# Optimization experiments

Hardware: AMD Instinct MI355X
Metric: run time of the kernel (lower is better)

The kernel has to match this reference:

```python
import jax, jax.numpy as jnp
import numpy as np

N_NODES, D, B, NEG2, DRUG_NUM = 20000, 512, 2048, 64, 2000
H1, H2 = 128, 64


def setup_inputs() -> dict:
    ks = jax.random.split(jax.random.key(0), 10)
    embed = jax.random.normal(ks[0], (N_NODES, D), dtype=jnp.float32)
    h = jax.random.randint(ks[1], (B, 1), 0, DRUG_NUM)
    t = jax.random.randint(ks[2], (B, 1), 0, N_NODES)
    n_s = jax.random.randint(ks[3], (B, NEG2), 0, DRUG_NUM)  # all < drug_num -> chunk branch
    s1 = 1.0 / np.sqrt(2 * D)
    s2 = 1.0 / np.sqrt(H1)
    s3 = 1.0 / np.sqrt(H2)
    W1 = jax.random.uniform(ks[4], (2 * D, H1), minval=-s1, maxval=s1, dtype=jnp.float32)
    b1 = jax.random.uniform(ks[5], (H1,), minval=-s1, maxval=s1, dtype=jnp.float32)
    W2 = jax.random.uniform(ks[6], (H1, H2), minval=-s2, maxval=s2, dtype=jnp.float32)
    b2 = jax.random.uniform(ks[7], (H2,), minval=-s2, maxval=s2, dtype=jnp.float32)
    W3 = jax.random.uniform(ks[8], (H2, 1), minval=-s3, maxval=s3, dtype=jnp.float32)
    b3 = jax.random.uniform(ks[9], (1,), minval=-s3, maxval=s3, dtype=jnp.float32)
    return {"embed": embed, "W1": W1, "b1": b1, "W2": W2, "b2": b2, "W3": W3, "b3": b3,
            "h": h, "t": t, "n_s": n_s}


def _mlp(x, W1, b1, W2, b2, W3, b3):
    # [..., 2D] -> [...] score
    x = jax.nn.relu(x @ W1 + b1)
    x = jax.nn.relu(x @ W2 + b2)
    return (x @ W3 + b3)[..., 0]


def reference(embed, W1, b1, W2, b2, W3, b3, h, t, n_s):
    K = n_s.shape[1] // 2
    n_t, n_h = n_s[:, :K], n_s[:, K:]
    h_e = embed[h]          # [B, 1, D]
    t_e = embed[t]          # [B, T, D]
    T = t.shape[1]
    # positive pairs: [B, T]
    pos = _mlp(jnp.concatenate([jnp.tile(h_e, (1, T, 1)), t_e], axis=-1),
               W1, b1, W2, b2, W3, b3)
    # corrupted-tail negatives: [B, K]
    neg1 = _mlp(jnp.concatenate([jnp.tile(h_e, (1, K, 1)), embed[n_t]], axis=-1),
                W1, b1, W2, b2, W3, b3)
    # corrupted-head negatives: [B, T*K] (T=1 here)
    neg2 = _mlp(jnp.concatenate([embed[n_h], jnp.tile(t_e, (1, K, 1))], axis=-1),
                W1, b1, W2, b2, W3, b3)
    neg = jnp.concatenate([neg1, neg2], axis=1)  # [B, 2K]
    return pos, neg
```

## Files before the change

kernel.cpp:

```cpp
#include <hip/hip_runtime.h>

#define DIM    512
#define BATCH  2048
#define NDRUG  2000
#define H1     128
#define H2     64
#define NITEM  65
#define SLAB   774144
#define W2F_OFF  (SLAB)
#define W1F_OFF  (W2F_OFF + 4096)
#define LP       65

typedef __attribute__((ext_vector_type(8))) short short8;
typedef __attribute__((ext_vector_type(4))) float floatx4;

__device__ inline unsigned f2bf(float x) {
    union { float f; unsigned u; } v; v.f = x;
    unsigned r = v.u + 0x7fffu + ((v.u >> 16) & 1u);
    return r >> 16;
}
__device__ inline unsigned pkbf(float a, float b) {
    return f2bf(a) | (f2bf(b) << 16);
}
__device__ inline short8 cvt8(const float* __restrict__ src) {
    float4 a = *(const float4*)src, b = *(const float4*)(src + 4);
    union { short8 s; unsigned u[4]; } v;
    v.u[0] = pkbf(a.x, a.y); v.u[1] = pkbf(a.z, a.w);
    v.u[2] = pkbf(b.x, b.y); v.u[3] = pkbf(b.z, b.w);
    return v.s;
}

__global__ __launch_bounds__(256) void pack_w(
    const float* __restrict__ W1, const float* __restrict__ W2,
    float* __restrict__ ws)
{
    const int blk = blockIdx.x, tid = threadIdx.x;
    if (blk < 64) {
        short8* W1f = (short8*)(ws + W1F_OFF);
        int item = blk * 256 + tid;
        int frag = item >> 6, lane = item & 63;
        int half = frag >> 7, kt = (frag >> 3) & 15, nt = frag & 7;
        int n = lane & 15, q = lane >> 4;
        short8 v;
        #pragma unroll
        for (int j = 0; j < 8; ++j) {
            int k = half * DIM + kt * 32 + q * 8 + j;
            v[j] = (short)f2bf(W1[k * H1 + nt * 16 + n]);
        }
        W1f[item] = v;
    } else {
        short8* W2f = (short8*)(ws + W2F_OFF);
        #pragma unroll
        for (int i = 0; i < 4; ++i) {
            int item = i * 256 + tid;
            int frag = item >> 6, lane = item & 63;
            int kt = frag >> 2, nt = frag & 3;
            int n = lane & 15, q = lane >> 4;
            short8 v;
            #pragma unroll
            for (int j = 0; j < 8; ++j)
                v[j] = (short)f2bf(W2[(kt * 32 + q * 8 + j) * H2 + nt * 16 + n]);
            W2f[item] = v;
        }
    }
}

__global__ __launch_bounds__(256) void layer1(
    const float* __restrict__ embed, const float* __restrict__ b1,
    const int* __restrict__ t, float* __restrict__ ws)
{
    __shared__ short8 ldsA[16 * LP];
    const short8* W1f = (const short8*)(ws + W1F_OFF);
    const int blk = blockIdx.x, tid = threadIdx.x;
    const bool isPQ = blk < 125;
    const int rowbase = isPQ ? blk * 16 : (blk - 125) * 16;

    #pragma unroll
    for (int i = 0; i < 4; ++i) {
        int u = i * 256 + tid;
        int r = u >> 6, c = u & 63;
        size_t grow = isPQ ? (size_t)(rowbase + r) : (size_t)t[rowbase + r];
        ldsA[r * LP + c] = cvt8(embed + grow * DIM + c * 8);
    }
    __syncthreads();

    const int lane = tid & 63, wv = tid >> 6;
    const int n = lane & 15, q = lane >> 4;

    if (isPQ) {
        const int T0 = wv * 4;
        const int half = (T0 >= 8) ? 1 : 0;
        floatx4 acc[4];
        #pragma unroll
        for (int i = 0; i < 4; ++i) acc[i] = (floatx4){0.f, 0.f, 0.f, 0.f};
        #pragma unroll
        for (int kt = 0; kt < 16; ++kt) {
            short8 a = ldsA[n * LP + kt * 4 + q];
            #pragma unroll
            for (int i = 0; i < 4; ++i) {
                int nt = (T0 + i) & 7;
                short8 bf = W1f[(size_t)(((half * 16 + kt) * 8) + nt) * 64 + lane];
                acc[i] = __builtin_amdgcn_mfma_f32_16x16x32_bf16(a, bf, acc[i], 0, 0, 0);
            }
        }
        float* tbl = ws + (half ? NDRUG * H1 : 0);
        #pragma unroll
        for (int i = 0; i < 4; ++i) {
            int nt = (T0 + i) & 7;
            float badd = half ? b1[nt * 16 + n] : 0.f;
            #pragma unroll
            for (int reg = 0; reg < 4; ++reg)
                tbl[(size_t)(rowbase + q * 4 + reg) * H1 + nt * 16 + n] =
                    acc[i][reg] + badd;
        }
    } else {
        const int T0 = wv * 2;
        floatx4 acc[2];
        #pragma unroll
        for (int i = 0; i < 2; ++i) acc[i] = (floatx4){0.f, 0.f, 0.f, 0.f};
        #pragma unroll
        for (int kt = 0; kt < 16; ++kt) {
            short8 a = ldsA[n * LP + kt * 4 + q];
            #pragma unroll
            for (int i = 0; i < 2; ++i) {
                int nt = T0 + i;
                short8 bf = W1f[(size_t)(((16 + kt) * 8) + nt) * 64 + lane];
                acc[i] = __builtin_amdgcn_mfma_f32_16x16x32_bf16(a, bf, acc[i], 0, 0, 0);
            }
        }
        float* tbl = ws + 2 * (NDRUG * H1);
        #pragma unroll
        for (int i = 0; i < 2; ++i) {
            int nt = T0 + i;
            float badd = b1[nt * 16 + n];
            #pragma unroll
            for (int reg = 0; reg < 4; ++reg)
                tbl[(size_t)(rowbase + q * 4 + reg) * H1 + nt * 16 + n] =
                    acc[i][reg] + badd;
        }
    }
}

__global__ __launch_bounds__(256) void score_mfma(
    const float* __restrict__ ws,
    const float* __restrict__ b2, const float* __restrict__ W3,
    const float* __restrict__ b3,
    const int* __restrict__ h, const int* __restrict__ ns,
    float* __restrict__ out)
{
    const float* P  = ws;
    const float* Q  = ws + NDRUG * H1;
    const float* Qt = Q + NDRUG * H1;
    const short8* W2f = (const short8*)(ws + W2F_OFF);

    const int lane = threadIdx.x & 63;
    const int wv   = threadIdx.x >> 6;
    const int tile = blockIdx.x * 4 + wv;
    const int n = lane & 15, q = lane >> 4;

    const int sg   = tile * 16 + n;
    const int b    = sg / NITEM;
    const int item = sg - b * NITEM;
    const float *Pr, *Qr;
    if (item == 0)       { Pr = P + h[b] * H1;                        Qr = Qt + b * H1; }
    else if (item <= 32) { Pr = P + h[b] * H1;                        Qr = Q + ns[b * 64 + item - 1] * H1; }
    else                 { Pr = P + ns[b * 64 + 32 + item - 33] * H1; Qr = Qt + b * H1; }

    floatx4 acc[4];
    #pragma unroll
    for (int nt = 0; nt < 4; ++nt) acc[nt] = (floatx4){0.f, 0.f, 0.f, 0.f};

    #pragma unroll
    for (int kt = 0; kt < 4; ++kt) {
        const int kb = kt * 32 + q * 8;
        float4 p0 = *(const float4*)(Pr + kb);
        float4 p1 = *(const float4*)(Pr + kb + 4);
        float4 q0 = *(const float4*)(Qr + kb);
        float4 q1 = *(const float4*)(Qr + kb + 4);
        union { short8 s; unsigned u[4]; } A;
        A.u[0] = pkbf(fmaxf(p0.x + q0.x, 0.f), fmaxf(p0.y + q0.y, 0.f));
        A.u[1] = pkbf(fmaxf(p0.z + q0.z, 0.f), fmaxf(p0.w + q0.w, 0.f));
        A.u[2] = pkbf(fmaxf(p1.x + q1.x, 0.f), fmaxf(p1.y + q1.y, 0.f));
        A.u[3] = pkbf(fmaxf(p1.z + q1.z, 0.f), fmaxf(p1.w + q1.w, 0.f));
        #pragma unroll
        for (int nt = 0; nt < 4; ++nt) {
            short8 bf = W2f[(kt * 4 + nt) * 64 + lane];
            acc[nt] = __builtin_amdgcn_mfma_f32_16x16x32_bf16(A.s, bf, acc[nt], 0, 0, 0);
        }
    }

    float part[4];
    #pragma unroll
    for (int reg = 0; reg < 4; ++reg) {
        float sum = 0.f;
        #pragma unroll
        for (int nt = 0; nt < 4; ++nt) {
            int j = nt * 16 + n;
            sum = fmaf(fmaxf(acc[nt][reg] + b2[j], 0.f), W3[j], sum);
        }
        part[reg] = sum;
    }
    #pragma unroll
    for (int m = 1; m < 16; m <<= 1) {
        #pragma unroll
        for (int reg = 0; reg < 4; ++reg)
            part[reg] += __shfl_xor(part[reg], m, 64);
    }
    if (n == 0) {
        const float base3 = b3[0];
        #pragma unroll
        for (int reg = 0; reg < 4; ++reg) {
            int gid = tile * 16 + q * 4 + reg;
            int bb  = gid / NITEM;
            int it  = gid - bb * NITEM;
            float val = part[reg] + base3;
            if (it == 0) out[bb] = val;
            else         out[BATCH + bb * 64 + (it - 1)] = val;
        }
    }
}

extern "C" void kernel_launch(void* const* d_in, const int* in_sizes, int n_in,
                              void* d_out, int out_size, void* d_ws, size_t ws_size,
                              hipStream_t stream) {
    const float* embed = (const float*)d_in[0];
    const float* W1    = (const float*)d_in[1];
    const float* b1    = (const float*)d_in[2];
    const float* W2    = (const float*)d_in[3];
    const float* b2    = (const float*)d_in[4];
    const float* W3    = (const float*)d_in[5];
    const float* b3    = (const float*)d_in[6];
    const int*   h     = (const int*)d_in[7];
    const int*   t     = (const int*)d_in[8];
    const int*   ns    = (const int*)d_in[9];
    float* out = (float*)d_out;
    float* ws  = (float*)d_ws;

    pack_w<<<65, 256, 0, stream>>>(W1, W2, ws);
    layer1<<<253, 256, 0, stream>>>(embed, b1, t, ws);
    score_mfma<<<(BATCH * NITEM) / 64, 256, 0, stream>>>(ws, b2, W3, b3,
                                                         h, ns, out);
}
```

Baseline: 117.5 us.

## Fuse three kernels into one cooperative kernel with grid-wide syncs

Merges the weight-packing, layer-1 table and scoring kernels into a single cooperative launch of 512 blocks that uses grid.sync() between the stages, and loops the scoring tiles persistently across blocks. The goal is to remove two kernel launch boundaries and their gaps. In exchange it adds grid-barrier cost and caps parallelism at 512 blocks for the scoring stage. If the cooperative launch fails, it falls back to the original three-kernel path.

```diff
diff --git a/kernel.cpp b/kernel.cpp
--- a/kernel.cpp
+++ b/kernel.cpp
@@ -1,4 +1,7 @@
 #include <hip/hip_runtime.h>
+#include <hip/hip_cooperative_groups.h>
+
+namespace cg = cooperative_groups;
 
 #define DIM    512
 #define BATCH  2048
@@ -10,6 +13,7 @@
 #define W2F_OFF  (SLAB)
 #define W1F_OFF  (W2F_OFF + 4096)
 #define LP       65
+#define GRID     512
 
 typedef __attribute__((ext_vector_type(8))) short short8;
 typedef __attribute__((ext_vector_type(4))) float floatx4;
@@ -30,50 +34,50 @@
     return v.s;
 }
 
-__global__ __launch_bounds__(256) void pack_w(
+
+__device__ inline void pack_w_body(int blk, int tid,
     const float* __restrict__ W1, const float* __restrict__ W2,
     float* __restrict__ ws)
 {
-    const int blk = blockIdx.x, tid = threadIdx.x;
     if (blk < 64) {
         short8* W1f = (short8*)(ws + W1F_OFF);
         int item = blk * 256 + tid;
-        int frag = item >> 6, lane = item & 63;
+        int frag = item >> 6, fl = item & 63;
         int half = frag >> 7, kt = (frag >> 3) & 15, nt = frag & 7;
-        int n = lane & 15, q = lane >> 4;
+        int fn = fl & 15, fq = fl >> 4;
         short8 v;
         #pragma unroll
         for (int j = 0; j < 8; ++j) {
-            int k = half * DIM + kt * 32 + q * 8 + j;
-            v[j] = (short)f2bf(W1[k * H1 + nt * 16 + n]);
+            int k = half * DIM + kt * 32 + fq * 8 + j;
+            v[j] = (short)f2bf(W1[k * H1 + nt * 16 + fn]);
         }
         W1f[item] = v;
-    } else {
+    } else if (blk == 64) {
         short8* W2f = (short8*)(ws + W2F_OFF);
         #pragma unroll
         for (int i = 0; i < 4; ++i) {
             int item = i * 256 + tid;
-            int frag = item >> 6, lane = item & 63;
+            int frag = item >> 6, fl = item & 63;
             int kt = frag >> 2, nt = frag & 3;
-            int n = lane & 15, q = lane >> 4;
+            int fn = fl & 15, fq = fl >> 4;
             short8 v;
             #pragma unroll
             for (int j = 0; j < 8; ++j)
-                v[j] = (short)f2bf(W2[(kt * 32 + q * 8 + j) * H2 + nt * 16 + n]);
+                v[j] = (short)f2bf(W2[(kt * 32 + fq * 8 + j) * H2 + nt * 16 + fn]);
             W2f[item] = v;
         }
     }
 }
 
-__global__ __launch_bounds__(256) void layer1(
+__device__ inline void layer1_body(int blk, int tid, short8* ldsA,
     const float* __restrict__ embed, const float* __restrict__ b1,
     const int* __restrict__ t, float* __restrict__ ws)
 {
-    __shared__ short8 ldsA[16 * LP];
     const short8* W1f = (const short8*)(ws + W1F_OFF);
-    const int blk = blockIdx.x, tid = threadIdx.x;
     const bool isPQ = blk < 125;
     const int rowbase = isPQ ? blk * 16 : (blk - 125) * 16;
+    const int lane = tid & 63, wv = tid >> 6;
+    const int n = lane & 15, q = lane >> 4;
 
     #pragma unroll
     for (int i = 0; i < 4; ++i) {
@@ -84,9 +88,6 @@
     }
     __syncthreads();
 
-    const int lane = tid & 63, wv = tid >> 6;
-    const int n = lane & 15, q = lane >> 4;
-
     if (isPQ) {
         const int T0 = wv * 4;
         const int half = (T0 >= 8) ? 1 : 0;
@@ -141,7 +142,7 @@
     }
 }
 
-__global__ __launch_bounds__(256) void score_mfma(
+__device__ inline void score_tile(int tile, int lane,
     const float* __restrict__ ws,
     const float* __restrict__ b2, const float* __restrict__ W3,
     const float* __restrict__ b3,
@@ -152,10 +153,6 @@
     const float* Q  = ws + NDRUG * H1;
     const float* Qt = Q + NDRUG * H1;
     const short8* W2f = (const short8*)(ws + W2F_OFF);
-
-    const int lane = threadIdx.x & 63;
-    const int wv   = threadIdx.x >> 6;
-    const int tile = blockIdx.x * 4 + wv;
     const int n = lane & 15, q = lane >> 4;
 
     const int sg   = tile * 16 + n;
@@ -218,6 +215,55 @@
             else         out[BATCH + bb * 64 + (it - 1)] = val;
         }
     }
+}
+
+__global__ __launch_bounds__(256, 2) void fused(
+    const float* __restrict__ embed, const float* __restrict__ W1,
+    const float* __restrict__ b1, const float* __restrict__ W2,
+    const float* __restrict__ b2, const float* __restrict__ W3,
+    const float* __restrict__ b3, const int* __restrict__ h,
+    const int* __restrict__ t, const int* __restrict__ ns,
+    float* __restrict__ ws, float* __restrict__ out)
+{
+    cg::grid_group grid = cg::this_grid();
+    __shared__ short8 ldsA[16 * LP];
+    const int blk = blockIdx.x, tid = threadIdx.x;
+
+    pack_w_body(blk, tid, W1, W2, ws);
+    grid.sync();
+
+    if (blk < 253) layer1_body(blk, tid, ldsA, embed, b1, t, ws);
+    grid.sync();
+
+    const int lane = tid & 63, wv = tid >> 6;
+    for (int job = blk; job < 2080; job += GRID)
+        score_tile(job * 4 + wv, lane, ws, b2, W3, b3, h, ns, out);
+}
+
+__global__ __launch_bounds__(256) void pack_w_k(
+    const float* __restrict__ W1, const float* __restrict__ W2,
+    float* __restrict__ ws)
+{
+    pack_w_body(blockIdx.x, threadIdx.x, W1, W2, ws);
+}
+
+__global__ __launch_bounds__(256) void layer1_k(
+    const float* __restrict__ embed, const float* __restrict__ b1,
+    const int* __restrict__ t, float* __restrict__ ws)
+{
+    __shared__ short8 ldsA[16 * LP];
+    layer1_body(blockIdx.x, threadIdx.x, ldsA, embed, b1, t, ws);
+}
+
+__global__ __launch_bounds__(256) void score_k(
+    const float* __restrict__ ws,
+    const float* __restrict__ b2, const float* __restrict__ W3,
+    const float* __restrict__ b3,
+    const int* __restrict__ h, const int* __restrict__ ns,
+    float* __restrict__ out)
+{
+    score_tile(blockIdx.x * 4 + (threadIdx.x >> 6), threadIdx.x & 63,
+               ws, b2, W3, b3, h, ns, out);
 }
 
 extern "C" void kernel_launch(void* const* d_in, const int* in_sizes, int n_in,
@@ -236,8 +282,16 @@
     float* out = (float*)d_out;
     float* ws  = (float*)d_ws;
 
-    pack_w<<<65, 256, 0, stream>>>(W1, W2, ws);
-    layer1<<<253, 256, 0, stream>>>(embed, b1, t, ws);
-    score_mfma<<<(BATCH * NITEM) / 64, 256, 0, stream>>>(ws, b2, W3, b3,
-                                                         h, ns, out);
-}
+    void* kargs[] = { (void*)&embed, (void*)&W1, (void*)&b1, (void*)&W2,
+                      (void*)&b2, (void*)&W3, (void*)&b3, (void*)&h,
+                      (void*)&t, (void*)&ns, (void*)&ws, (void*)&out };
+    hipError_t err = hipLaunchCooperativeKernel((void*)fused, dim3(GRID),
+                                                dim3(256), kargs, 0, stream);
+    if (err != hipSuccess) {
+        (void)hipGetLastError();
+        pack_w_k<<<65, 256, 0, stream>>>(W1, W2, ws);
+        layer1_k<<<253, 256, 0, stream>>>(embed, b1, t, ws);
+        score_k<<<(BATCH * NITEM) / 64, 256, 0, stream>>>(ws, b2, W3, b3,
+                                                          h, ns, out);
+    }
+}
```

Result: slower. 224.4 us (+91.0%).

## Reorder W1 fragments, double-buffer weight loads, stage W2 in LDS, batch gathers

Applied to the files above, without the earlier changes.

Changes the packed W1 layout so each wave's fragments for a column tile are contiguous along K. Layer 1 now prefetches the next group of W1 fragments into registers while it issues MFMAs on the current group. The score kernel copies the packed W2 fragments into shared memory once per block and issues all P/Q row gathers before the MFMA loop. Together these aim to hide global load latency, at the cost of more registers and an extra block-wide barrier plus 16KB of LDS per score block.

```diff
diff --git a/kernel.cpp b/kernel.cpp
--- a/kernel.cpp
+++ b/kernel.cpp
@@ -38,14 +38,15 @@
     if (blk < 64) {
         short8* W1f = (short8*)(ws + W1F_OFF);
         int item = blk * 256 + tid;
-        int frag = item >> 6, lane = item & 63;
-        int half = frag >> 7, kt = (frag >> 3) & 15, nt = frag & 7;
-        int n = lane & 15, q = lane >> 4;
+        int frag = item >> 6, fl = item & 63;
+        int half = frag >> 7, rem = frag & 127;
+        int nt = rem >> 4, kt = rem & 15;
+        int fn = fl & 15, fq = fl >> 4;
         short8 v;
         #pragma unroll
         for (int j = 0; j < 8; ++j) {
-            int k = half * DIM + kt * 32 + q * 8 + j;
-            v[j] = (short)f2bf(W1[k * H1 + nt * 16 + n]);
+            int k = half * DIM + kt * 32 + fq * 8 + j;
+            v[j] = (short)f2bf(W1[k * H1 + nt * 16 + fn]);
         }
         W1f[item] = v;
     } else {
@@ -53,19 +54,52 @@
         #pragma unroll
         for (int i = 0; i < 4; ++i) {
             int item = i * 256 + tid;
-            int frag = item >> 6, lane = item & 63;
+            int frag = item >> 6, fl = item & 63;
             int kt = frag >> 2, nt = frag & 3;
-            int n = lane & 15, q = lane >> 4;
+            int fn = fl & 15, fq = fl >> 4;
             short8 v;
             #pragma unroll
             for (int j = 0; j < 8; ++j)
-                v[j] = (short)f2bf(W2[(kt * 32 + q * 8 + j) * H2 + nt * 16 + n]);
+                v[j] = (short)f2bf(W2[(kt * 32 + fq * 8 + j) * H2 + nt * 16 + fn]);
             W2f[item] = v;
         }
     }
 }
 
-__global__ __launch_bounds__(256) void layer1(
+template<int NT>
+__device__ inline void l1_core(const short8* __restrict__ Wh,
+                               const short8* __restrict__ ldsA,
+                               int n, int q, int lane, floatx4* acc)
+{
+    short8 B[2][NT * 4];
+    #pragma unroll
+    for (int i = 0; i < NT; ++i)
+        #pragma unroll
+        for (int k = 0; k < 4; ++k)
+            B[0][i * 4 + k] = Wh[(i * 16 + k) * 64 + lane];
+
+    #pragma unroll
+    for (int g = 0; g < 4; ++g) {
+        const int cur = g & 1, nxt = cur ^ 1;
+        if (g < 3) {
+            #pragma unroll
+            for (int i = 0; i < NT; ++i)
+                #pragma unroll
+                for (int k = 0; k < 4; ++k)
+                    B[nxt][i * 4 + k] = Wh[(i * 16 + (g + 1) * 4 + k) * 64 + lane];
+        }
+        #pragma unroll
+        for (int k = 0; k < 4; ++k) {
+            short8 a = ldsA[n * LP + (g * 4 + k) * 4 + q];
+            #pragma unroll
+            for (int i = 0; i < NT; ++i)
+                acc[i] = __builtin_amdgcn_mfma_f32_16x16x32_bf16(
+                             a, B[cur][i * 4 + k], acc[i], 0, 0, 0);
+        }
+    }
+}
+
+__global__ __launch_bounds__(256) void layer1_k(
     const float* __restrict__ embed, const float* __restrict__ b1,
     const int* __restrict__ t, float* __restrict__ ws)
 {
@@ -74,6 +108,8 @@
     const int blk = blockIdx.x, tid = threadIdx.x;
     const bool isPQ = blk < 125;
     const int rowbase = isPQ ? blk * 16 : (blk - 125) * 16;
+    const int lane = tid & 63, wv = tid >> 6;
+    const int n = lane & 15, q = lane >> 4;
 
     #pragma unroll
     for (int i = 0; i < 4; ++i) {
@@ -84,29 +120,19 @@
     }
     __syncthreads();
 
-    const int lane = tid & 63, wv = tid >> 6;
-    const int n = lane & 15, q = lane >> 4;
-
     if (isPQ) {
         const int T0 = wv * 4;
         const int half = (T0 >= 8) ? 1 : 0;
+        const int ntbase = T0 & 7;
         floatx4 acc[4];
         #pragma unroll
         for (int i = 0; i < 4; ++i) acc[i] = (floatx4){0.f, 0.f, 0.f, 0.f};
-        #pragma unroll
-        for (int kt = 0; kt < 16; ++kt) {
-            short8 a = ldsA[n * LP + kt * 4 + q];
-            #pragma unroll
-            for (int i = 0; i < 4; ++i) {
-                int nt = (T0 + i) & 7;
-                short8 bf = W1f[(size_t)(((half * 16 + kt) * 8) + nt) * 64 + lane];
-                acc[i] = __builtin_amdgcn_mfma_f32_16x16x32_bf16(a, bf, acc[i], 0, 0, 0);
-            }
-        }
+        const short8* Wh = W1f + (size_t)((half * 8 + ntbase) * 16) * 64;
+        l1_core<4>(Wh, ldsA, n, q, lane, acc);
         float* tbl = ws + (half ? NDRUG * H1 : 0);
         #pragma unroll
         for (int i = 0; i < 4; ++i) {
-            int nt = (T0 + i) & 7;
+            int nt = ntbase + i;
             float badd = half ? b1[nt * 16 + n] : 0.f;
             #pragma unroll
             for (int reg = 0; reg < 4; ++reg)
@@ -114,24 +140,16 @@
                     acc[i][reg] + badd;
         }
     } else {
-        const int T0 = wv * 2;
+        const int ntbase = wv * 2;
         floatx4 acc[2];
         #pragma unroll
         for (int i = 0; i < 2; ++i) acc[i] = (floatx4){0.f, 0.f, 0.f, 0.f};
-        #pragma unroll
-        for (int kt = 0; kt < 16; ++kt) {
-            short8 a = ldsA[n * LP + kt * 4 + q];
-            #pragma unroll
-            for (int i = 0; i < 2; ++i) {
-                int nt = T0 + i;
-                short8 bf = W1f[(size_t)(((16 + kt) * 8) + nt) * 64 + lane];
-                acc[i] = __builtin_amdgcn_mfma_f32_16x16x32_bf16(a, bf, acc[i], 0, 0, 0);
-            }
-        }
+        const short8* Wh = W1f + (size_t)((8 + ntbase) * 16) * 64;
+        l1_core<2>(Wh, ldsA, n, q, lane, acc);
         float* tbl = ws + 2 * (NDRUG * H1);
         #pragma unroll
         for (int i = 0; i < 2; ++i) {
-            int nt = T0 + i;
+            int nt = ntbase + i;
             float badd = b1[nt * 16 + n];
             #pragma unroll
             for (int reg = 0; reg < 4; ++reg)
@@ -141,42 +159,57 @@
     }
 }
 
-__global__ __launch_bounds__(256) void score_mfma(
+__global__ __launch_bounds__(256) void score_k(
     const float* __restrict__ ws,
     const float* __restrict__ b2, const float* __restrict__ W3,
     const float* __restrict__ b3,
     const int* __restrict__ h, const int* __restrict__ ns,
     float* __restrict__ out)
 {
+    __shared__ short8 w2lds[1024];
     const float* P  = ws;
     const float* Q  = ws + NDRUG * H1;
     const float* Qt = Q + NDRUG * H1;
     const short8* W2f = (const short8*)(ws + W2F_OFF);
 
-    const int lane = threadIdx.x & 63;
-    const int wv   = threadIdx.x >> 6;
+    const int tid = threadIdx.x;
+    const int lane = tid & 63, wv = tid >> 6;
     const int tile = blockIdx.x * 4 + wv;
     const int n = lane & 15, q = lane >> 4;
 
     const int sg   = tile * 16 + n;
     const int b    = sg / NITEM;
     const int item = sg - b * NITEM;
-    const float *Pr, *Qr;
-    if (item == 0)       { Pr = P + h[b] * H1;                        Qr = Qt + b * H1; }
-    else if (item <= 32) { Pr = P + h[b] * H1;                        Qr = Q + ns[b * 64 + item - 1] * H1; }
-    else                 { Pr = P + ns[b * 64 + 32 + item - 33] * H1; Qr = Qt + b * H1; }
-
-    floatx4 acc[4];
-    #pragma unroll
-    for (int nt = 0; nt < 4; ++nt) acc[nt] = (floatx4){0.f, 0.f, 0.f, 0.f};
-
+    const bool midQ = (item >= 1 && item <= 32);
+    const int rowA = (item <= 32) ? h[b] : ns[b * 64 + 32 + (item - 33)];
+    const int rowB = midQ ? ns[b * 64 + item - 1] : b;
+
+    #pragma unroll
+    for (int i = 0; i < 4; ++i)
+        w2lds[i * 256 + tid] = W2f[i * 256 + tid];
+    __syncthreads();
+
+    const float* Pr = P + (size_t)rowA * H1;
+    const float* Qr = (midQ ? Q : Qt) + (size_t)rowB * H1;
+
+    float4 pr[8], qr[8];
     #pragma unroll
     for (int kt = 0; kt < 4; ++kt) {
         const int kb = kt * 32 + q * 8;
-        float4 p0 = *(const float4*)(Pr + kb);
-        float4 p1 = *(const float4*)(Pr + kb + 4);
-        float4 q0 = *(const float4*)(Qr + kb);
-        float4 q1 = *(const float4*)(Qr + kb + 4);
+        pr[kt * 2]     = *(const float4*)(Pr + kb);
+        pr[kt * 2 + 1] = *(const float4*)(Pr + kb + 4);
+        qr[kt * 2]     = *(const float4*)(Qr + kb);
+        qr[kt * 2 + 1] = *(const float4*)(Qr + kb + 4);
+    }
+
+    floatx4 acc[4];
+    #pragma unroll
+    for (int nt = 0; nt < 4; ++nt) acc[nt] = (floatx4){0.f, 0.f, 0.f, 0.f};
+
+    #pragma unroll
+    for (int kt = 0; kt < 4; ++kt) {
+        float4 p0 = pr[kt * 2], p1 = pr[kt * 2 + 1];
+        float4 q0 = qr[kt * 2], q1 = qr[kt * 2 + 1];
         union { short8 s; unsigned u[4]; } A;
         A.u[0] = pkbf(fmaxf(p0.x + q0.x, 0.f), fmaxf(p0.y + q0.y, 0.f));
         A.u[1] = pkbf(fmaxf(p0.z + q0.z, 0.f), fmaxf(p0.w + q0.w, 0.f));
@@ -184,7 +217,7 @@
         A.u[3] = pkbf(fmaxf(p1.z + q1.z, 0.f), fmaxf(p1.w + q1.w, 0.f));
         #pragma unroll
         for (int nt = 0; nt < 4; ++nt) {
-            short8 bf = W2f[(kt * 4 + nt) * 64 + lane];
+            short8 bf = w2lds[(kt * 4 + nt) * 64 + lane];
             acc[nt] = __builtin_amdgcn_mfma_f32_16x16x32_bf16(A.s, bf, acc[nt], 0, 0, 0);
         }
     }
@@ -237,7 +270,7 @@
     float* ws  = (float*)d_ws;
 
     pack_w<<<65, 256, 0, stream>>>(W1, W2, ws);
-    layer1<<<253, 256, 0, stream>>>(embed, b1, t, ws);
-    score_mfma<<<(BATCH * NITEM) / 64, 256, 0, stream>>>(ws, b2, W3, b3,
-                                                         h, ns, out);
-}
+    layer1_k<<<253, 256, 0, stream>>>(embed, b1, t, ws);
+    score_k<<<(BATCH * NITEM) / 64, 256, 0, stream>>>(ws, b2, W3, b3,
+                                                      h, ns, out);
+}
```

Measured after the change: 114.6 us (median of 2 runs). 2.4% less time.
